# Performance work log

Measured on AMD Instinct MI355X. Metric: run time of the kernel, lower is better.

The kernel has to match this reference:

```python
import math
import jax, jax.numpy as jnp
import numpy as np

B, S, D, H = 128, 512, 768, 12
DH = D // H  # 64


def setup_inputs() -> dict:
    key = jax.random.key(0)
    k1, k2, k3, k4, k5 = jax.random.split(key, 5)
    return {
        "X": jax.random.normal(k1, (B, S, D), jnp.float32),
        "W_qkv": jax.random.normal(k2, (3 * D, D), jnp.float32) * 0.02,
        "b_qkv": jax.random.normal(k3, (3 * D,), jnp.float32) * 0.02,
        "W_dense": jax.random.normal(k4, (D, D), jnp.float32) * 0.02,
        "b_dense": jax.random.normal(k5, (D,), jnp.float32) * 0.02,
    }


def reference(X, W_qkv, b_qkv, W_dense, b_dense):
    # Faithful translation of SelfAttention.forward (including its unusual
    # seq/batch layout: scores are [S*H, B, B] and the tril mask FILLS the
    # lower triangle with -10000, exactly as masked_fill_(tril, -1e4) does).
    b, s, d = X.shape
    qkv = jnp.einsum('bsd,ed->bse', X, W_qkv) + b_qkv            # [B,S,3D]
    qkv = qkv.reshape(b, s, H, 3 * DH)
    q = qkv[..., :DH]
    k = qkv[..., DH:2 * DH]
    v = qkv[..., 2 * DH:]
    q = q.reshape(b, s * H, DH).transpose(1, 0, 2)               # [S*H,B,DH]
    k = k.reshape(b, s * H, DH).transpose(1, 0, 2)
    v = v.reshape(b, s * H, DH).transpose(1, 0, 2)
    scores = jnp.einsum('nbd,ncd->nbc', q, k) / math.sqrt(DH)    # [S*H,B,B]
    scores = scores.reshape(s, H, b, b)
    tril = jnp.tril(jnp.ones((s, b, b), bool))[:, None]          # [S,1,B,B]
    scores = jnp.where(tril, jnp.float32(-10000.0), scores)
    probs = jax.nn.softmax(scores, axis=-1).reshape(s * H, b, b)
    ctx = jnp.einsum('nbc,ncd->nbd', probs, v)                   # [S*H,B,DH]
    ctx = ctx.reshape(s, H, b, DH).transpose(2, 0, 1, 3).reshape(b, s, d)
    out = jnp.einsum('bsd,ed->bse', ctx, W_dense)                # bias NOT added
    return (out, b_dense)
```

## Files before the change

### kernel.cpp

```cpp
#include <hip/hip_runtime.h>
#include <hip/hip_bf16.h>
#include <cstdint>
#include <cstddef>


typedef __attribute__((ext_vector_type(8))) short bf16x8_t;
typedef __attribute__((ext_vector_type(4))) float f32x4_t;

__device__ inline unsigned short f2bf(float x) {
  union { float f; unsigned int u; } v; v.f = x;
  return (unsigned short)((v.u + 0x7FFFu + ((v.u >> 16) & 1u)) >> 16);
}

#define GLL16(gp, lp) __builtin_amdgcn_global_load_lds(                      \
    (const __attribute__((address_space(1))) void*)(gp),                     \
    (__attribute__((address_space(3))) void*)(lp), 16, 0, 0)

__global__ __launch_bounds__(256) void cvt_kernel(const float* __restrict__ in,
                                                  unsigned short* __restrict__ out,
                                                  int n4) {
  int i = blockIdx.x * 256 + threadIdx.x;
  if (i >= n4) return;
  const float4 v = ((const float4*)in)[i];
  ushort4 o;
  o.x = f2bf(v.x); o.y = f2bf(v.y); o.z = f2bf(v.z); o.w = f2bf(v.w);
  ((ushort4*)out)[i] = o;
}

__global__ void bias_tail(const float* __restrict__ b, float* __restrict__ out) {
  int i = blockIdx.x * 256 + threadIdx.x;
  if (i < 768) out[(size_t)128 * 512 * 768 + i] = b[i];
}

__global__ __launch_bounds__(256) void gemm_qkv(
    const unsigned short* __restrict__ A,
    const unsigned short* __restrict__ Bt,
    const float* __restrict__ bias,
    unsigned short* __restrict__ Qb,
    unsigned short* __restrict__ Kb,
    unsigned short* __restrict__ Vb) {
  __shared__ unsigned short As[128 * 32];
  __shared__ unsigned short Bs[128 * 32];
  const int tid = threadIdx.x;
  const int wave = tid >> 6, lane = tid & 63;
  const int lane15 = lane & 15, quad = lane >> 4;
  const int mBase = blockIdx.y * 128;
  const int nBase = blockIdx.x * 128;
  const int wm = (wave >> 1) * 64;
  const int wn = (wave & 1) * 64;

  f32x4_t acc[4][4];
#pragma unroll
  for (int i = 0; i < 4; ++i)
#pragma unroll
    for (int j = 0; j < 4; ++j) { f32x4_t z = {0.f, 0.f, 0.f, 0.f}; acc[i][j] = z; }

  const int srow = wave * 32 + (lane >> 2);
  const int kcol = (lane & 3) * 8;
  const unsigned short* Ag = A + (size_t)(mBase + srow) * 768 + kcol;
  const unsigned short* Bg = Bt + (size_t)(nBase + srow) * 768 + kcol;
  unsigned short* lA = &As[(wave * 32) * 32];
  unsigned short* lB = &Bs[(wave * 32) * 32];

  for (int k0 = 0; k0 < 768; k0 += 32) {
    GLL16(Ag + k0, lA);
    GLL16(Ag + 16 * 768 + k0, lA + 16 * 32);
    GLL16(Bg + k0, lB);
    GLL16(Bg + 16 * 768 + k0, lB + 16 * 32);
    __syncthreads();
    bf16x8_t aF[4], bF[4];
#pragma unroll
    for (int im = 0; im < 4; ++im)
      aF[im] = *(const bf16x8_t*)&As[(wm + im * 16 + lane15) * 32 + quad * 8];
#pragma unroll
    for (int in = 0; in < 4; ++in)
      bF[in] = *(const bf16x8_t*)&Bs[(wn + in * 16 + lane15) * 32 + quad * 8];
#pragma unroll
    for (int im = 0; im < 4; ++im)
#pragma unroll
      for (int in = 0; in < 4; ++in)
        acc[im][in] = __builtin_amdgcn_mfma_f32_16x16x32_bf16(aF[im], bF[in], acc[im][in], 0, 0, 0);
    __syncthreads();
  }

#pragma unroll
  for (int in = 0; in < 4; ++in) {
    const int e = nBase + wn + in * 16 + lane15;
    const float bv = bias[e];
    const int h = e / 192;
    const int c = e - h * 192;
    const int sec = c >> 6;
    const int dh = c & 63;
    unsigned short* dst = (sec == 0) ? Qb : ((sec == 1) ? Kb : Vb);
#pragma unroll
    for (int im = 0; im < 4; ++im) {
#pragma unroll
      for (int r = 0; r < 4; ++r) {
        const int m = mBase + wm + im * 16 + quad * 4 + r;
        const int bb = m >> 9;
        const int ss = m & 511;
        dst[(size_t)((ss * 12 + h) * 128 + bb) * 64 + dh] = f2bf(acc[im][in][r] + bv);
      }
    }
  }
}

__global__ __launch_bounds__(256) void attn_kernel(
    const unsigned short* __restrict__ Qg,
    const unsigned short* __restrict__ Kg,
    const unsigned short* __restrict__ Vg,
    unsigned short* __restrict__ Ctx) {
  __shared__ unsigned short Qs[128 * 64];
  __shared__ unsigned short Ks[128 * 64];
  __shared__ unsigned short Vt[64 * 128];
  __shared__ unsigned short Ps[4][16 * 128];

  const int n = blockIdx.x;
  const int s = n / 12;
  const int h = n - s * 12;
  const int tid = threadIdx.x;
  const int wave = tid >> 6, lane = tid & 63;
  const int lane15 = lane & 15, quad = lane >> 4;
  const size_t base = (size_t)n * 8192;

  {
    const uint4* q4 = (const uint4*)(Qg + base);
    const uint4* k4 = (const uint4*)(Kg + base);
    uint4* qs4 = (uint4*)Qs;
    uint4* ks4 = (uint4*)Ks;
#pragma unroll
    for (int i = 0; i < 4; ++i) {
      qs4[tid + i * 256] = q4[tid + i * 256];
      ks4[tid + i * 256] = k4[tid + i * 256];
    }
    const unsigned short* vg = Vg + base;
#pragma unroll
    for (int ii = 0; ii < 32; ++ii) {
      int i = tid + ii * 256;
      int c = i >> 6, dh = i & 63;
      Vt[dh * 128 + c] = vg[i];
    }
  }
  __syncthreads();

  f32x4_t sc[2][8];
#pragma unroll
  for (int im = 0; im < 2; ++im)
#pragma unroll
    for (int in = 0; in < 8; ++in) { f32x4_t z = {0.f, 0.f, 0.f, 0.f}; sc[im][in] = z; }

#pragma unroll
  for (int kk = 0; kk < 2; ++kk) {
    bf16x8_t a0 = *(const bf16x8_t*)&Qs[(wave * 32 + lane15) * 64 + kk * 32 + quad * 8];
    bf16x8_t a1 = *(const bf16x8_t*)&Qs[(wave * 32 + 16 + lane15) * 64 + kk * 32 + quad * 8];
#pragma unroll
    for (int in = 0; in < 8; ++in) {
      bf16x8_t b = *(const bf16x8_t*)&Ks[(in * 16 + lane15) * 64 + kk * 32 + quad * 8];
      sc[0][in] = __builtin_amdgcn_mfma_f32_16x16x32_bf16(a0, b, sc[0][in], 0, 0, 0);
      sc[1][in] = __builtin_amdgcn_mfma_f32_16x16x32_bf16(a1, b, sc[1][in], 0, 0, 0);
    }
  }

  unsigned short* myP = &Ps[wave][0];

#pragma unroll 1
  for (int im = 0; im < 2; ++im) {
#pragma unroll
    for (int r = 0; r < 4; ++r) {
      const int row = wave * 32 + im * 16 + quad * 4 + r;
      float vals[8];
      float mx = -3.0e38f;
#pragma unroll
      for (int in = 0; in < 8; ++in) {
        const int col = in * 16 + lane15;
        float v = sc[im][in][r] * 0.125f;
        v = (col <= row) ? -10000.0f : v;
        vals[in] = v;
        mx = fmaxf(mx, v);
      }
      mx = fmaxf(mx, __shfl_xor(mx, 1, 16));
      mx = fmaxf(mx, __shfl_xor(mx, 2, 16));
      mx = fmaxf(mx, __shfl_xor(mx, 4, 16));
      mx = fmaxf(mx, __shfl_xor(mx, 8, 16));
      float sum = 0.f;
#pragma unroll
      for (int in = 0; in < 8; ++in) {
        const float e_ = __expf(vals[in] - mx);
        vals[in] = e_;
        sum += e_;
      }
      sum += __shfl_xor(sum, 1, 16);
      sum += __shfl_xor(sum, 2, 16);
      sum += __shfl_xor(sum, 4, 16);
      sum += __shfl_xor(sum, 8, 16);
      const float inv = 1.0f / sum;
#pragma unroll
      for (int in = 0; in < 8; ++in)
        myP[(quad * 4 + r) * 128 + in * 16 + lane15] = f2bf(vals[in] * inv);
    }
    __syncthreads();

    f32x4_t oc[4];
#pragma unroll
    for (int nt = 0; nt < 4; ++nt) { f32x4_t z = {0.f, 0.f, 0.f, 0.f}; oc[nt] = z; }
#pragma unroll
    for (int kk = 0; kk < 4; ++kk) {
      bf16x8_t a = *(const bf16x8_t*)&myP[lane15 * 128 + kk * 32 + quad * 8];
#pragma unroll
      for (int nt = 0; nt < 4; ++nt) {
        bf16x8_t b = *(const bf16x8_t*)&Vt[(nt * 16 + lane15) * 128 + kk * 32 + quad * 8];
        oc[nt] = __builtin_amdgcn_mfma_f32_16x16x32_bf16(a, b, oc[nt], 0, 0, 0);
      }
    }
#pragma unroll
    for (int nt = 0; nt < 4; ++nt) {
#pragma unroll
      for (int r = 0; r < 4; ++r) {
        const int bb = wave * 32 + im * 16 + quad * 4 + r;
        Ctx[((size_t)bb * 512 + s) * 768 + h * 64 + nt * 16 + lane15] = f2bf(oc[nt][r]);
      }
    }
    __syncthreads();
  }
}

__global__ __launch_bounds__(256) void gemm_out(
    const unsigned short* __restrict__ A,
    const unsigned short* __restrict__ Bt,
    float* __restrict__ Out) {
  __shared__ unsigned short As[128 * 32];
  __shared__ unsigned short Bs[128 * 32];
  const int tid = threadIdx.x;
  const int wave = tid >> 6, lane = tid & 63;
  const int lane15 = lane & 15, quad = lane >> 4;
  const int mBase = blockIdx.y * 128;
  const int nBase = blockIdx.x * 128;
  const int wm = (wave >> 1) * 64;
  const int wn = (wave & 1) * 64;

  f32x4_t acc[4][4];
#pragma unroll
  for (int i = 0; i < 4; ++i)
#pragma unroll
    for (int j = 0; j < 4; ++j) { f32x4_t z = {0.f, 0.f, 0.f, 0.f}; acc[i][j] = z; }

  const int srow = wave * 32 + (lane >> 2);
  const int kcol = (lane & 3) * 8;
  const unsigned short* Ag = A + (size_t)(mBase + srow) * 768 + kcol;
  const unsigned short* Bg = Bt + (size_t)(nBase + srow) * 768 + kcol;
  unsigned short* lA = &As[(wave * 32) * 32];
  unsigned short* lB = &Bs[(wave * 32) * 32];

  for (int k0 = 0; k0 < 768; k0 += 32) {
    GLL16(Ag + k0, lA);
    GLL16(Ag + 16 * 768 + k0, lA + 16 * 32);
    GLL16(Bg + k0, lB);
    GLL16(Bg + 16 * 768 + k0, lB + 16 * 32);
    __syncthreads();
    bf16x8_t aF[4], bF[4];
#pragma unroll
    for (int im = 0; im < 4; ++im)
      aF[im] = *(const bf16x8_t*)&As[(wm + im * 16 + lane15) * 32 + quad * 8];
#pragma unroll
    for (int in = 0; in < 4; ++in)
      bF[in] = *(const bf16x8_t*)&Bs[(wn + in * 16 + lane15) * 32 + quad * 8];
#pragma unroll
    for (int im = 0; im < 4; ++im)
#pragma unroll
      for (int in = 0; in < 4; ++in)
        acc[im][in] = __builtin_amdgcn_mfma_f32_16x16x32_bf16(aF[im], bF[in], acc[im][in], 0, 0, 0);
    __syncthreads();
  }

#pragma unroll
  for (int in = 0; in < 4; ++in) {
    const int e = nBase + wn + in * 16 + lane15;
#pragma unroll
    for (int im = 0; im < 4; ++im)
#pragma unroll
      for (int r = 0; r < 4; ++r) {
        const int m = mBase + wm + im * 16 + quad * 4 + r;
        Out[(size_t)m * 768 + e] = acc[im][in][r];
      }
  }
}

extern "C" void kernel_launch(void* const* d_in, const int* in_sizes, int n_in,
                              void* d_out, int out_size, void* d_ws, size_t ws_size,
                              hipStream_t stream) {
  const float* X    = (const float*)d_in[0];
  const float* Wqkv = (const float*)d_in[1];
  const float* bqkv = (const float*)d_in[2];
  const float* Wd   = (const float*)d_in[3];
  const float* bd   = (const float*)d_in[4];
  float* out = (float*)d_out;

  char* ws = (char*)d_ws;
  unsigned short* Xb  = (unsigned short*)(ws);
  unsigned short* Qb  = (unsigned short*)(ws + 100663296);
  unsigned short* Kb  = (unsigned short*)(ws + 201326592);
  unsigned short* Vb  = (unsigned short*)(ws + 301989888);
  unsigned short* Wqb = (unsigned short*)(ws + 402653184);
  unsigned short* Wdb = (unsigned short*)(ws + 406192128);

  cvt_kernel<<<dim3(49152), 256, 0, stream>>>(X, Xb, 12582912);
  cvt_kernel<<<dim3(1728), 256, 0, stream>>>(Wqkv, Wqb, 442368);
  cvt_kernel<<<dim3(576), 256, 0, stream>>>(Wd, Wdb, 147456);
  bias_tail<<<dim3(3), 256, 0, stream>>>(bd, out);

  gemm_qkv<<<dim3(18, 512), 256, 0, stream>>>(Xb, Wqb, bqkv, Qb, Kb, Vb);
  attn_kernel<<<dim3(6144), 256, 0, stream>>>(Qb, Kb, Vb, Xb );
  gemm_out<<<dim3(6, 512), 256, 0, stream>>>(Xb, Wdb, out);
}
```

Measured before the change: 1.288 ms.

## Store QKV row-major, gather per-head in attention, and pad LDS tiles

The QKV GEMM now writes one row-major [B*S, 2304] buffer instead of scattering 2-byte elements into transposed per-head Q/K/V arrays. The attention kernel gathers its strided rows with 16-byte loads and builds the V transpose from vector loads. LDS rows are padded (72/136) to avoid bank conflicts, and the GEMM LDS staging is reordered so fragments are read contiguously per lane. The cost moves from scattered GEMM stores to strided attention loads, and the padding uses more LDS per block.

New measurement: 1.260 ms. 2.2% less time.

```diff
diff --git a/kernel.cpp b/kernel.cpp
--- a/kernel.cpp
+++ b/kernel.cpp
@@ -36,9 +36,7 @@
     const unsigned short* __restrict__ A,
     const unsigned short* __restrict__ Bt,
     const float* __restrict__ bias,
-    unsigned short* __restrict__ Qb,
-    unsigned short* __restrict__ Kb,
-    unsigned short* __restrict__ Vb) {
+    unsigned short* __restrict__ QKV) {
   __shared__ unsigned short As[128 * 32];
   __shared__ unsigned short Bs[128 * 32];
   const int tid = threadIdx.x;
@@ -55,26 +53,27 @@
 #pragma unroll
     for (int j = 0; j < 4; ++j) { f32x4_t z = {0.f, 0.f, 0.f, 0.f}; acc[i][j] = z; }
 
-  const int srow = wave * 32 + (lane >> 2);
-  const int kcol = (lane & 3) * 8;
-  const unsigned short* Ag = A + (size_t)(mBase + srow) * 768 + kcol;
-  const unsigned short* Bg = Bt + (size_t)(nBase + srow) * 768 + kcol;
-  unsigned short* lA = &As[(wave * 32) * 32];
-  unsigned short* lB = &Bs[(wave * 32) * 32];
+  const int r16 = lane & 15;
+  const int ck8 = (lane >> 4) * 8;
+  const unsigned short* Ag = A + (size_t)(mBase + wave * 32 + r16) * 768 + ck8;
+  const unsigned short* Bg = Bt + (size_t)(nBase + wave * 32 + r16) * 768 + ck8;
+  unsigned short* lA = &As[wave * 1024];
+  unsigned short* lB = &Bs[wave * 1024];
+
+  const int aOff = ((wave >> 1) * 4) * 512 + lane * 8;
+  const int bOff = ((wave & 1) * 4) * 512 + lane * 8;
 
   for (int k0 = 0; k0 < 768; k0 += 32) {
     GLL16(Ag + k0, lA);
-    GLL16(Ag + 16 * 768 + k0, lA + 16 * 32);
+    GLL16(Ag + 16 * 768 + k0, lA + 512);
     GLL16(Bg + k0, lB);
-    GLL16(Bg + 16 * 768 + k0, lB + 16 * 32);
+    GLL16(Bg + 16 * 768 + k0, lB + 512);
     __syncthreads();
     bf16x8_t aF[4], bF[4];
 #pragma unroll
-    for (int im = 0; im < 4; ++im)
-      aF[im] = *(const bf16x8_t*)&As[(wm + im * 16 + lane15) * 32 + quad * 8];
-#pragma unroll
-    for (int in = 0; in < 4; ++in)
-      bF[in] = *(const bf16x8_t*)&Bs[(wn + in * 16 + lane15) * 32 + quad * 8];
+    for (int im = 0; im < 4; ++im) aF[im] = *(const bf16x8_t*)&As[aOff + im * 512];
+#pragma unroll
+    for (int in = 0; in < 4; ++in) bF[in] = *(const bf16x8_t*)&Bs[bOff + in * 512];
 #pragma unroll
     for (int im = 0; im < 4; ++im)
 #pragma unroll
@@ -83,37 +82,30 @@
     __syncthreads();
   }
 
-#pragma unroll
-  for (int in = 0; in < 4; ++in) {
-    const int e = nBase + wn + in * 16 + lane15;
-    const float bv = bias[e];
-    const int h = e / 192;
-    const int c = e - h * 192;
-    const int sec = c >> 6;
-    const int dh = c & 63;
-    unsigned short* dst = (sec == 0) ? Qb : ((sec == 1) ? Kb : Vb);
-#pragma unroll
-    for (int im = 0; im < 4; ++im) {
-#pragma unroll
-      for (int r = 0; r < 4; ++r) {
-        const int m = mBase + wm + im * 16 + quad * 4 + r;
-        const int bb = m >> 9;
-        const int ss = m & 511;
-        dst[(size_t)((ss * 12 + h) * 128 + bb) * 64 + dh] = f2bf(acc[im][in][r] + bv);
-      }
+  float bv[4];
+#pragma unroll
+  for (int in = 0; in < 4; ++in) bv[in] = bias[nBase + wn + in * 16 + lane15];
+
+#pragma unroll
+  for (int im = 0; im < 4; ++im) {
+#pragma unroll
+    for (int r = 0; r < 4; ++r) {
+      const int m = mBase + wm + im * 16 + quad * 4 + r;
+      unsigned short* orow = QKV + (size_t)m * 2304 + nBase + wn + lane15;
+#pragma unroll
+      for (int in = 0; in < 4; ++in)
+        orow[in * 16] = f2bf(acc[im][in][r] + bv[in]);
     }
   }
 }
 
 __global__ __launch_bounds__(256) void attn_kernel(
-    const unsigned short* __restrict__ Qg,
-    const unsigned short* __restrict__ Kg,
-    const unsigned short* __restrict__ Vg,
+    const unsigned short* __restrict__ QKV,
     unsigned short* __restrict__ Ctx) {
-  __shared__ unsigned short Qs[128 * 64];
-  __shared__ unsigned short Ks[128 * 64];
-  __shared__ unsigned short Vt[64 * 128];
-  __shared__ unsigned short Ps[4][16 * 128];
+  __shared__ unsigned short Qs[128 * 72];
+  __shared__ unsigned short Ks[128 * 72];
+  __shared__ unsigned short Vt[64 * 136];
+  __shared__ unsigned short Ps[4][16 * 136];
 
   const int n = blockIdx.x;
   const int s = n / 12;
@@ -121,24 +113,25 @@
   const int tid = threadIdx.x;
   const int wave = tid >> 6, lane = tid & 63;
   const int lane15 = lane & 15, quad = lane >> 4;
-  const size_t base = (size_t)n * 8192;
-
+
+#pragma unroll
+  for (int it = 0; it < 4; ++it) {
+    const int idx = it * 256 + tid;
+    const int bb = idx >> 3, seg = idx & 7;
+    const size_t g = (size_t)(bb * 512 + s) * 2304 + h * 192 + seg * 8;
+    *(uint4*)&Qs[bb * 72 + seg * 8] = *(const uint4*)&QKV[g];
+    *(uint4*)&Ks[bb * 72 + seg * 8] = *(const uint4*)&QKV[g + 64];
+  }
   {
-    const uint4* q4 = (const uint4*)(Qg + base);
-    const uint4* k4 = (const uint4*)(Kg + base);
-    uint4* qs4 = (uint4*)Qs;
-    uint4* ks4 = (uint4*)Ks;
-#pragma unroll
-    for (int i = 0; i < 4; ++i) {
-      qs4[tid + i * 256] = q4[tid + i * 256];
-      ks4[tid + i * 256] = k4[tid + i * 256];
-    }
-    const unsigned short* vg = Vg + base;
-#pragma unroll
-    for (int ii = 0; ii < 32; ++ii) {
-      int i = tid + ii * 256;
-      int c = i >> 6, dh = i & 63;
-      Vt[dh * 128 + c] = vg[i];
+    const int c = tid & 127, half = tid >> 7;
+    const size_t vb = (size_t)(c * 512 + s) * 2304 + h * 192 + 128;
+#pragma unroll
+    for (int dd = 0; dd < 4; ++dd) {
+      const int dseg = half * 4 + dd;
+      uint4 v = *(const uint4*)&QKV[vb + dseg * 8];
+      const unsigned short* pv = (const unsigned short*)&v;
+#pragma unroll
+      for (int j = 0; j < 8; ++j) Vt[(dseg * 8 + j) * 136 + c] = pv[j];
     }
   }
   __syncthreads();
@@ -151,11 +144,11 @@
 
 #pragma unroll
   for (int kk = 0; kk < 2; ++kk) {
-    bf16x8_t a0 = *(const bf16x8_t*)&Qs[(wave * 32 + lane15) * 64 + kk * 32 + quad * 8];
-    bf16x8_t a1 = *(const bf16x8_t*)&Qs[(wave * 32 + 16 + lane15) * 64 + kk * 32 + quad * 8];
+    bf16x8_t a0 = *(const bf16x8_t*)&Qs[(wave * 32 + lane15) * 72 + kk * 32 + quad * 8];
+    bf16x8_t a1 = *(const bf16x8_t*)&Qs[(wave * 32 + 16 + lane15) * 72 + kk * 32 + quad * 8];
 #pragma unroll
     for (int in = 0; in < 8; ++in) {
-      bf16x8_t b = *(const bf16x8_t*)&Ks[(in * 16 + lane15) * 64 + kk * 32 + quad * 8];
+      bf16x8_t b = *(const bf16x8_t*)&Ks[(in * 16 + lane15) * 72 + kk * 32 + quad * 8];
       sc[0][in] = __builtin_amdgcn_mfma_f32_16x16x32_bf16(a0, b, sc[0][in], 0, 0, 0);
       sc[1][in] = __builtin_amdgcn_mfma_f32_16x16x32_bf16(a1, b, sc[1][in], 0, 0, 0);
     }
@@ -196,7 +189,7 @@
       const float inv = 1.0f / sum;
 #pragma unroll
       for (int in = 0; in < 8; ++in)
-        myP[(quad * 4 + r) * 128 + in * 16 + lane15] = f2bf(vals[in] * inv);
+        myP[(quad * 4 + r) * 136 + in * 16 + lane15] = f2bf(vals[in] * inv);
     }
     __syncthreads();
 
@@ -205,10 +198,10 @@
     for (int nt = 0; nt < 4; ++nt) { f32x4_t z = {0.f, 0.f, 0.f, 0.f}; oc[nt] = z; }
 #pragma unroll
     for (int kk = 0; kk < 4; ++kk) {
-      bf16x8_t a = *(const bf16x8_t*)&myP[lane15 * 128 + kk * 32 + quad * 8];
+      bf16x8_t a = *(const bf16x8_t*)&myP[lane15 * 136 + kk * 32 + quad * 8];
 #pragma unroll
       for (int nt = 0; nt < 4; ++nt) {
-        bf16x8_t b = *(const bf16x8_t*)&Vt[(nt * 16 + lane15) * 128 + kk * 32 + quad * 8];
+        bf16x8_t b = *(const bf16x8_t*)&Vt[(nt * 16 + lane15) * 136 + kk * 32 + quad * 8];
         oc[nt] = __builtin_amdgcn_mfma_f32_16x16x32_bf16(a, b, oc[nt], 0, 0, 0);
       }
     }
@@ -244,26 +237,27 @@
 #pragma unroll
     for (int j = 0; j < 4; ++j) { f32x4_t z = {0.f, 0.f, 0.f, 0.f}; acc[i][j] = z; }
 
-  const int srow = wave * 32 + (lane >> 2);
-  const int kcol = (lane & 3) * 8;
-  const unsigned short* Ag = A + (size_t)(mBase + srow) * 768 + kcol;
-  const unsigned short* Bg = Bt + (size_t)(nBase + srow) * 768 + kcol;
-  unsigned short* lA = &As[(wave * 32) * 32];
-  unsigned short* lB = &Bs[(wave * 32) * 32];
+  const int r16 = lane & 15;
+  const int ck8 = (lane >> 4) * 8;
+  const unsigned short* Ag = A + (size_t)(mBase + wave * 32 + r16) * 768 + ck8;
+  const unsigned short* Bg = Bt + (size_t)(nBase + wave * 32 + r16) * 768 + ck8;
+  unsigned short* lA = &As[wave * 1024];
+  unsigned short* lB = &Bs[wave * 1024];
+
+  const int aOff = ((wave >> 1) * 4) * 512 + lane * 8;
+  const int bOff = ((wave & 1) * 4) * 512 + lane * 8;
 
   for (int k0 = 0; k0 < 768; k0 += 32) {
     GLL16(Ag + k0, lA);
-    GLL16(Ag + 16 * 768 + k0, lA + 16 * 32);
+    GLL16(Ag + 16 * 768 + k0, lA + 512);
     GLL16(Bg + k0, lB);
-    GLL16(Bg + 16 * 768 + k0, lB + 16 * 32);
+    GLL16(Bg + 16 * 768 + k0, lB + 512);
     __syncthreads();
     bf16x8_t aF[4], bF[4];
 #pragma unroll
-    for (int im = 0; im < 4; ++im)
-      aF[im] = *(const bf16x8_t*)&As[(wm + im * 16 + lane15) * 32 + quad * 8];
-#pragma unroll
-    for (int in = 0; in < 4; ++in)
-      bF[in] = *(const bf16x8_t*)&Bs[(wn + in * 16 + lane15) * 32 + quad * 8];
+    for (int im = 0; im < 4; ++im) aF[im] = *(const bf16x8_t*)&As[aOff + im * 512];
+#pragma unroll
+    for (int in = 0; in < 4; ++in) bF[in] = *(const bf16x8_t*)&Bs[bOff + in * 512];
 #pragma unroll
     for (int im = 0; im < 4; ++im)
 #pragma unroll
@@ -273,15 +267,15 @@
   }
 
 #pragma unroll
-  for (int in = 0; in < 4; ++in) {
-    const int e = nBase + wn + in * 16 + lane15;
-#pragma unroll
-    for (int im = 0; im < 4; ++im)
-#pragma unroll
-      for (int r = 0; r < 4; ++r) {
-        const int m = mBase + wm + im * 16 + quad * 4 + r;
-        Out[(size_t)m * 768 + e] = acc[im][in][r];
-      }
+  for (int im = 0; im < 4; ++im) {
+#pragma unroll
+    for (int r = 0; r < 4; ++r) {
+      const int m = mBase + wm + im * 16 + quad * 4 + r;
+      float* orow = Out + (size_t)m * 768 + nBase + wn + lane15;
+#pragma unroll
+      for (int in = 0; in < 4; ++in)
+        orow[in * 16] = acc[im][in][r];
+    }
   }
 }
 
@@ -297,9 +291,7 @@
 
   char* ws = (char*)d_ws;
   unsigned short* Xb  = (unsigned short*)(ws);
-  unsigned short* Qb  = (unsigned short*)(ws + 100663296);
-  unsigned short* Kb  = (unsigned short*)(ws + 201326592);
-  unsigned short* Vb  = (unsigned short*)(ws + 301989888);
+  unsigned short* QKV = (unsigned short*)(ws + 100663296);
   unsigned short* Wqb = (unsigned short*)(ws + 402653184);
   unsigned short* Wdb = (unsigned short*)(ws + 406192128);
 
@@ -308,7 +300,7 @@
   cvt_kernel<<<dim3(576), 256, 0, stream>>>(Wd, Wdb, 147456);
   bias_tail<<<dim3(3), 256, 0, stream>>>(bd, out);
 
-  gemm_qkv<<<dim3(18, 512), 256, 0, stream>>>(Xb, Wqb, bqkv, Qb, Kb, Vb);
-  attn_kernel<<<dim3(6144), 256, 0, stream>>>(Qb, Kb, Vb, Xb );
+  gemm_qkv<<<dim3(18, 512), 256, 0, stream>>>(Xb, Wqb, bqkv, QKV);
+  attn_kernel<<<dim3(6144), 256, 0, stream>>>(QKV, Xb );
   gemm_out<<<dim3(6, 512), 256, 0, stream>>>(Xb, Wdb, out);
 }
```
